# Performance work log

Measured on AMD Instinct MI355X. Metric: run time of the kernel, lower is better.

Reference implementation:

```python
import jax, jax.numpy as jnp
import numpy as np
import math

B, N, D = 2, 2048, 512   # batch, seq, input_dim
H = 8                     # num_head
DK, DV = 512, 512         # dim_k, dim_v (dim_v == input_dim for the final reshape)


def setup_inputs() -> dict:
    key = jax.random.key(0)
    ks = jax.random.split(key, 7)
    s = 1.0 / math.sqrt(D)
    return {
        "x":  jax.random.normal(ks[0], (B, N, D), jnp.float32),
        "Wq": jax.random.normal(ks[1], (H, DK, D), jnp.float32) * s,
        "bq": jax.random.normal(ks[2], (H, DK), jnp.float32) * s,
        "Wk": jax.random.normal(ks[3], (DK, D), jnp.float32) * s,
        "bk": jax.random.normal(ks[4], (DK,), jnp.float32) * s,
        "Wv": jax.random.normal(ks[5], (DV, D), jnp.float32) * s,
        "bv": jax.random.normal(ks[6], (DV,), jnp.float32) * s,
    }


def reference(x, Wq, bq, Wk, bk, Wv, bv):
    # Per-head Q projections (each head projects to full dim_k), batched as one einsum.
    Q = jnp.einsum("bnd,hkd->bhnk", x, Wq) + bq[None, :, None, :]   # [B,H,N,DK]
    K = x @ Wk.T + bk                                               # [B,N,DK] (shared)
    V = x @ Wv.T + bv                                               # [B,N,DV] (shared)
    scores = jnp.einsum("bhnk,bmk->bhnm", Q, K) / math.sqrt(DK)     # [B,H,N,N]
    A = jax.nn.softmax(scores, axis=-1)                             # softmax over keys
    At = jnp.swapaxes(A, -2, -1)                                    # quirk: transpose before V matmul
    out = jnp.einsum("bhnm,bnv->bhmv", A, V)                        # == At @ V (V broadcast over heads)
    out = out.reshape(-1, N, D)                                     # [B*H, N, D] since DV == D
    return (At, out)
```

## Files before the change

### kernel.cpp

```cpp
#include <hip/hip_runtime.h>
#include <stdint.h>

typedef __attribute__((ext_vector_type(8))) short short8;
typedef __attribute__((ext_vector_type(4))) float f4;
typedef unsigned short u16;

#define Nn 2048
#define Dd 512
#define Hh 8
#define BNrows 4096
#define SCALE 0.044194173824159216f

__device__ __forceinline__ u16 f2b(float f) {
  union { float f; uint32_t u; } c; c.f = f;
  uint32_t u = c.u;
  u += 0x7fffu + ((u >> 16) & 1u);
  return (u16)(u >> 16);
}

__device__ __forceinline__ void gload_lds16(const void* g, void* l) {
  __builtin_amdgcn_global_load_lds((const __attribute__((address_space(1))) void*)g,
                                   (__attribute__((address_space(3))) void*)l, 16, 0, 0);
}

__global__ void prep_kernel(const float* __restrict__ x,  u16* __restrict__ xb,
                            const float* __restrict__ Wq, u16* __restrict__ Wqb,
                            const float* __restrict__ Wk, u16* __restrict__ Wkb,
                            const float* __restrict__ Wv, u16* __restrict__ Wvb,
                            float* __restrict__ ssum) {
  const int g = blockIdx.x * 256 + threadIdx.x;
  if (g >= 589824) {
    ssum[g - 589824] = 0.0f;
    return;
  }
  const float* src; u16* dst; int i;
  if (g < 262144)      { src = x;  dst = xb;  i = g; }
  else if (g < 524288) { src = Wq; dst = Wqb; i = g - 262144; }
  else if (g < 557056) { src = Wk; dst = Wkb; i = g - 524288; }
  else                 { src = Wv; dst = Wvb; i = g - 557056; }
  const f4* s4 = (const f4*)src;
  f4 a = s4[2*i], b = s4[2*i+1];
  short8 o;
  o[0]=(short)f2b(a[0]); o[1]=(short)f2b(a[1]); o[2]=(short)f2b(a[2]); o[3]=(short)f2b(a[3]);
  o[4]=(short)f2b(b[0]); o[5]=(short)f2b(b[1]); o[6]=(short)f2b(b[2]); o[7]=(short)f2b(b[3]);
  ((short8*)dst)[i] = o;
}

__global__ void recip_kernel(const float* __restrict__ s, float* __restrict__ rs, int n) {
  int i = blockIdx.x * 256 + threadIdx.x;
  if (i < n) rs[i] = 1.0f / s[i];
}

__launch_bounds__(256)
__global__ void proj_all(const u16* __restrict__ xb, const u16* __restrict__ Wqb,
                         const u16* __restrict__ Wkb, const u16* __restrict__ Wvb,
                         const float* __restrict__ bq, const float* __restrict__ bk,
                         const float* __restrict__ bv,
                         u16* __restrict__ Qb, u16* __restrict__ Kb, u16* __restrict__ Vtb) {
  __shared__ __align__(16) u16 Al[128*64];
  __shared__ __align__(16) u16 Bl[128*64];
  const int bid = blockIdx.x;
  const u16 *A, *Bm; u16* C;
  const float* bias;
  int lda, ldb, ldc, bias_row, m0, n0;
  if (bid < 1024) {
    A = xb; lda = 512; Bm = Wqb; ldb = 512; bias = bq; bias_row = 0;
    C = Qb; ldc = 4096; n0 = (bid & 31) * 128; m0 = (bid >> 5) * 128;
  } else if (bid < 1152) {
    const int id = bid - 1024;
    A = xb; lda = 512; Bm = Wkb; ldb = 512; bias = bk; bias_row = 0;
    C = Kb; ldc = 512; n0 = (id & 3) * 128; m0 = (id >> 2) * 128;
  } else {
    const int id = bid - 1152;
    A = Wvb; lda = 512; Bm = xb; ldb = 512; bias = bv; bias_row = 1;
    C = Vtb; ldc = 4096; n0 = (id & 31) * 128; m0 = (id >> 5) * 128;
  }
  const int t = threadIdx.x, w = t >> 6, l = t & 63;
  const int wm = (w >> 1) * 64, wn = (w & 1) * 64;
  const int srow = l >> 3, scol = (l & 7) * 8;
  f4 acc[4][4] = {};
  for (int k0 = 0; k0 < 512; k0 += 64) {
    #pragma unroll
    for (int j = 0; j < 4; ++j) {
      const int chunk = (w << 2) + j;
      const int row = (chunk << 3) + srow;
      gload_lds16(A  + (size_t)(m0 + row) * lda + (k0 + scol), &Al[chunk << 9]);
      gload_lds16(Bm + (size_t)(n0 + row) * ldb + (k0 + scol), &Bl[chunk << 9]);
    }
    __syncthreads();
    #pragma unroll
    for (int ks = 0; ks < 64; ks += 32) {
      short8 af[4], bfr[4];
      #pragma unroll
      for (int i = 0; i < 4; ++i)
        af[i] = *(const short8*)&Al[(wm + i*16 + (l & 15)) * 64 + ks + ((l >> 4) << 3)];
      #pragma unroll
      for (int j = 0; j < 4; ++j)
        bfr[j] = *(const short8*)&Bl[(wn + j*16 + (l & 15)) * 64 + ks + ((l >> 4) << 3)];
      #pragma unroll
      for (int i = 0; i < 4; ++i)
        #pragma unroll
        for (int j = 0; j < 4; ++j)
          acc[i][j] = __builtin_amdgcn_mfma_f32_16x16x32_bf16(af[i], bfr[j], acc[i][j], 0, 0, 0);
    }
    __syncthreads();
  }
  const int cr = (l >> 4) << 2, cc = l & 15;
  #pragma unroll
  for (int i = 0; i < 4; ++i) {
    #pragma unroll
    for (int j = 0; j < 4; ++j) {
      const int col = n0 + wn + j*16 + cc;
      #pragma unroll
      for (int r = 0; r < 4; ++r) {
        const int row = m0 + wm + i*16 + cr + r;
        const float bb = bias_row ? bias[row] : bias[col];
        C[(size_t)row * ldc + col] = f2b(acc[i][j][r] + bb);
      }
    }
  }
}

__launch_bounds__(256)
__global__ void score_gemm(const u16* __restrict__ Kb, const u16* __restrict__ Qb,
                           float* __restrict__ E, float* __restrict__ ssum) {
  __shared__ __align__(16) u16 Al[128*64];
  __shared__ __align__(16) u16 Bl[128*64];
  const int t = threadIdx.x, w = t >> 6, l = t & 63;
  const int bh = blockIdx.z, b = bh >> 3, h = bh & 7;
  const u16* A  = Kb + (size_t)b * Nn * Dd;
  const u16* Bm = Qb + (size_t)b * Nn * BNrows + h * Dd;
  float* C = E + (size_t)bh * Nn * Nn;
  const int m0 = blockIdx.y * 128, n0 = blockIdx.x * 128;
  const int wm = (w >> 1) * 64, wn = (w & 1) * 64;
  const int srow = l >> 3, scol = (l & 7) * 8;
  f4 acc[4][4] = {};
  for (int k0 = 0; k0 < 512; k0 += 64) {
    #pragma unroll
    for (int j = 0; j < 4; ++j) {
      const int chunk = (w << 2) + j;
      const int row = (chunk << 3) + srow;
      gload_lds16(A  + (size_t)(m0 + row) * Dd      + (k0 + scol), &Al[chunk << 9]);
      gload_lds16(Bm + (size_t)(n0 + row) * BNrows  + (k0 + scol), &Bl[chunk << 9]);
    }
    __syncthreads();
    #pragma unroll
    for (int ks = 0; ks < 64; ks += 32) {
      short8 af[4], bfr[4];
      #pragma unroll
      for (int i = 0; i < 4; ++i)
        af[i] = *(const short8*)&Al[(wm + i*16 + (l & 15)) * 64 + ks + ((l >> 4) << 3)];
      #pragma unroll
      for (int j = 0; j < 4; ++j)
        bfr[j] = *(const short8*)&Bl[(wn + j*16 + (l & 15)) * 64 + ks + ((l >> 4) << 3)];
      #pragma unroll
      for (int i = 0; i < 4; ++i)
        #pragma unroll
        for (int j = 0; j < 4; ++j)
          acc[i][j] = __builtin_amdgcn_mfma_f32_16x16x32_bf16(af[i], bfr[j], acc[i][j], 0, 0, 0);
    }
    __syncthreads();
  }
  const int cr = (l >> 4) << 2, cc = l & 15;
  float psum[4] = {0.f, 0.f, 0.f, 0.f};
  #pragma unroll
  for (int i = 0; i < 4; ++i) {
    #pragma unroll
    for (int j = 0; j < 4; ++j) {
      const int col = n0 + wn + j*16 + cc;
      #pragma unroll
      for (int r = 0; r < 4; ++r) {
        const int row = m0 + wm + i*16 + cr + r;
        const float e = __expf(acc[i][j][r] * SCALE);
        C[(size_t)row * Nn + col] = e;
        psum[j] += e;
      }
    }
  }
  float* sp = ssum + bh * Nn + n0 + wn;
  #pragma unroll
  for (int j = 0; j < 4; ++j) {
    float p = psum[j];
    p += __shfl_xor(p, 16);
    p += __shfl_xor(p, 32);
    if (l < 16) atomicAdd(&sp[j*16 + l], p);
  }
}

__launch_bounds__(256)
__global__ void out_gemm(float* __restrict__ E, const u16* __restrict__ Vt,
                         const float* __restrict__ rs, float* __restrict__ O) {
  __shared__ __align__(16) u16 Al[64*32];
  __shared__ __align__(16) u16 Bl[512*32];
  const int t = threadIdx.x, w = t >> 6, l = t & 63;
  const int mb = blockIdx.x, bh = blockIdx.y, b = bh >> 3;
  float* Ep = E + (size_t)bh * Nn * Nn + (size_t)mb * 64 * Nn;
  const float* rsp = rs + bh * Nn;
  const u16* Vp = Vt + (size_t)b * Nn;
  const int wv = w << 7;
  const int am = t >> 2, an8 = (t & 3) << 3;
  const int bvr = l >> 2, bcol = (l & 3) << 3;
  f4 acc[4][8] = {};
  for (int k0 = 0; k0 < Nn; k0 += 32) {
    #pragma unroll
    for (int j = 0; j < 8; ++j) {
      const int chunk = (w << 3) + j;
      const int vrow = (chunk << 4) + bvr;
      gload_lds16(Vp + (size_t)vrow * BNrows + k0 + bcol, &Bl[chunk << 9]);
    }
    float* ap = Ep + (size_t)am * Nn + k0 + an8;
    f4 x0 = *(const f4*)ap;
    f4 x1 = *(const f4*)(ap + 4);
    const f4 r0 = *(const f4*)(rsp + k0 + an8);
    const f4 r1 = *(const f4*)(rsp + k0 + an8 + 4);
    x0 *= r0; x1 *= r1;
    *(f4*)ap = x0; *(f4*)(ap + 4) = x1;
    short8 ab;
    ab[0]=(short)f2b(x0[0]); ab[1]=(short)f2b(x0[1]); ab[2]=(short)f2b(x0[2]); ab[3]=(short)f2b(x0[3]);
    ab[4]=(short)f2b(x1[0]); ab[5]=(short)f2b(x1[1]); ab[6]=(short)f2b(x1[2]); ab[7]=(short)f2b(x1[3]);
    *(short8*)&Al[am * 32 + an8] = ab;
    __syncthreads();
    short8 af[4];
    #pragma unroll
    for (int i = 0; i < 4; ++i)
      af[i] = *(const short8*)&Al[(i*16 + (l & 15)) * 32 + ((l >> 4) << 3)];
    #pragma unroll
    for (int j = 0; j < 8; ++j) {
      const short8 bfj = *(const short8*)&Bl[(wv + j*16 + (l & 15)) * 32 + ((l >> 4) << 3)];
      #pragma unroll
      for (int i = 0; i < 4; ++i)
        acc[i][j] = __builtin_amdgcn_mfma_f32_16x16x32_bf16(af[i], bfj, acc[i][j], 0, 0, 0);
    }
    __syncthreads();
  }
  float* Op = O + (size_t)bh * Nn * Dd + (size_t)mb * 64 * Dd;
  #pragma unroll
  for (int i = 0; i < 4; ++i)
    #pragma unroll
    for (int j = 0; j < 8; ++j)
      #pragma unroll
      for (int r = 0; r < 4; ++r)
        Op[(size_t)(i*16 + ((l >> 4) << 2) + r) * Dd + (wv + j*16 + (l & 15))] = acc[i][j][r];
}

extern "C" void kernel_launch(void* const* d_in, const int* in_sizes, int n_in,
                              void* d_out, int out_size, void* d_ws, size_t ws_size,
                              hipStream_t stream) {
  const float* x  = (const float*)d_in[0];
  const float* Wq = (const float*)d_in[1];
  const float* bq = (const float*)d_in[2];
  const float* Wk = (const float*)d_in[3];
  const float* bk = (const float*)d_in[4];
  const float* Wv = (const float*)d_in[5];
  const float* bv = (const float*)d_in[6];

  u16* xb  = (u16*)d_ws;
  u16* Wqb = xb  + (size_t)4096 * 512;
  u16* Wkb = Wqb + (size_t)4096 * 512;
  u16* Wvb = Wkb + (size_t)512 * 512;
  u16* Qb  = Wvb + (size_t)512 * 512;
  u16* Kb  = Qb  + (size_t)4096 * 4096;
  u16* Vtb = Kb  + (size_t)4096 * 512;
  float* ssum = (float*)(Vtb + (size_t)4096 * 512);
  float* rs   = ssum + 16 * 2048;

  float* Eo = (float*)d_out;
  float* Oo = Eo + (size_t)16 * 2048 * 2048;

  prep_kernel<<<2432, 256, 0, stream>>>(x, xb, Wq, Wqb, Wk, Wkb, Wv, Wvb, ssum);
  proj_all<<<1280, 256, 0, stream>>>(xb, Wqb, Wkb, Wvb, bq, bk, bv, Qb, Kb, Vtb);
  score_gemm<<<dim3(16, 16, 16), 256, 0, stream>>>(Kb, Qb, Eo, ssum);
  recip_kernel<<<128, 256, 0, stream>>>(ssum, rs, 32768);
  out_gemm<<<dim3(32, 16), 256, 0, stream>>>(Eo, Vtb, rs, Oo);
}
```

Before: 687.2 us.

## Double-buffer out_gemm V tiles, prefetch E rows, and XOR-swizzle LDS layouts

Rewrites the out_gemm main loop as a software pipeline. The next V tile loads asynchronously into a second LDS buffer, and the next E/rowsum registers are fetched while the current tile is normalized and fed to MFMA. Both A and B LDS tiles use an XOR swizzle to cut bank conflicts, and the V-transpose producer writes in the matching swizzled order. Explicit waitcnt/barrier/setprio control replaces __syncthreads. Costs are a doubled B LDS footprint and a launch-bounds occupancy hint, plus correctness risk from the hand-tuned vmcnt count.

```diff
diff --git a/kernel.cpp b/kernel.cpp
--- a/kernel.cpp
+++ b/kernel.cpp
@@ -115,7 +115,11 @@
       for (int r = 0; r < 4; ++r) {
         const int row = m0 + wm + i*16 + cr + r;
         const float bb = bias_row ? bias[row] : bias[col];
-        C[(size_t)row * ldc + col] = f2b(acc[i][j][r] + bb);
+        int colw = col;
+        if (bias_row) {
+          colw = (col & ~31) | ((((col >> 3) & 3) ^ ((row >> 1) & 3)) << 3) | (col & 7);
+        }
+        C[(size_t)row * ldc + colw] = f2b(acc[i][j][r] + bb);
       }
     }
   }
@@ -187,11 +191,11 @@
   }
 }
 
-__launch_bounds__(256)
+__launch_bounds__(256, 2)
 __global__ void out_gemm(float* __restrict__ E, const u16* __restrict__ Vt,
                          const float* __restrict__ rs, float* __restrict__ O) {
+  __shared__ __align__(16) u16 Bl[2][512*32];
   __shared__ __align__(16) u16 Al[64*32];
-  __shared__ __align__(16) u16 Bl[512*32];
   const int t = threadIdx.x, w = t >> 6, l = t & 63;
   const int mb = blockIdx.x, bh = blockIdx.y, b = bh >> 3;
   float* Ep = E + (size_t)bh * Nn * Nn + (size_t)mb * 64 * Nn;
@@ -199,40 +203,76 @@
   const u16* Vp = Vt + (size_t)b * Nn;
   const int wv = w << 7;
   const int am = t >> 2, an8 = (t & 3) << 3;
-  const int bvr = l >> 2, bcol = (l & 3) << 3;
+  const int bvr = l >> 2, bg8 = (l & 3) << 3;
   f4 acc[4][8] = {};
-  for (int k0 = 0; k0 < Nn; k0 += 32) {
+
+  f4 e0, e1, r0, r1, e0n, e1n, r0n, r1n;
+  #pragma unroll
+  for (int j = 0; j < 8; ++j) {
+    const int chunk = (w << 3) + j;
+    const int vrow = (chunk << 4) + bvr;
+    gload_lds16(Vp + (size_t)vrow * BNrows + bg8, &Bl[0][chunk << 9]);
+  }
+  {
+    const float* ap = Ep + (size_t)am * Nn + an8;
+    e0 = *(const f4*)ap; e1 = *(const f4*)(ap + 4);
+    r0 = *(const f4*)(rsp + an8); r1 = *(const f4*)(rsp + an8 + 4);
+  }
+
+  for (int it = 0; it < 64; ++it) {
+    const int cur = it & 1;
+    const int kn = (it < 63) ? ((it + 1) << 5) : (63 << 5);
     #pragma unroll
     for (int j = 0; j < 8; ++j) {
       const int chunk = (w << 3) + j;
       const int vrow = (chunk << 4) + bvr;
-      gload_lds16(Vp + (size_t)vrow * BNrows + k0 + bcol, &Bl[chunk << 9]);
-    }
-    float* ap = Ep + (size_t)am * Nn + k0 + an8;
-    f4 x0 = *(const f4*)ap;
-    f4 x1 = *(const f4*)(ap + 4);
-    const f4 r0 = *(const f4*)(rsp + k0 + an8);
-    const f4 r1 = *(const f4*)(rsp + k0 + an8 + 4);
-    x0 *= r0; x1 *= r1;
-    *(f4*)ap = x0; *(f4*)(ap + 4) = x1;
-    short8 ab;
-    ab[0]=(short)f2b(x0[0]); ab[1]=(short)f2b(x0[1]); ab[2]=(short)f2b(x0[2]); ab[3]=(short)f2b(x0[3]);
-    ab[4]=(short)f2b(x1[0]); ab[5]=(short)f2b(x1[1]); ab[6]=(short)f2b(x1[2]); ab[7]=(short)f2b(x1[3]);
-    *(short8*)&Al[am * 32 + an8] = ab;
-    __syncthreads();
-    short8 af[4];
-    #pragma unroll
-    for (int i = 0; i < 4; ++i)
-      af[i] = *(const short8*)&Al[(i*16 + (l & 15)) * 32 + ((l >> 4) << 3)];
+      gload_lds16(Vp + (size_t)vrow * BNrows + kn + bg8, &Bl[cur ^ 1][chunk << 9]);
+    }
+    {
+      const float* apn = Ep + (size_t)am * Nn + kn + an8;
+      e0n = *(const f4*)apn; e1n = *(const f4*)(apn + 4);
+      r0n = *(const f4*)(rsp + kn + an8); r1n = *(const f4*)(rsp + kn + an8 + 4);
+    }
+    {
+      f4 x0 = e0 * r0, x1 = e1 * r1;
+      float* ap = Ep + (size_t)am * Nn + (it << 5) + an8;
+      *(f4*)ap = x0; *(f4*)(ap + 4) = x1;
+      short8 ab;
+      ab[0]=(short)f2b(x0[0]); ab[1]=(short)f2b(x0[1]); ab[2]=(short)f2b(x0[2]); ab[3]=(short)f2b(x0[3]);
+      ab[4]=(short)f2b(x1[0]); ab[5]=(short)f2b(x1[1]); ab[6]=(short)f2b(x1[2]); ab[7]=(short)f2b(x1[3]);
+      const int ag = (t & 3) ^ ((am >> 1) & 3);
+      *(short8*)&Al[am * 32 + (ag << 3)] = ab;
+    }
+    asm volatile("s_waitcnt lgkmcnt(0)" ::: "memory");
+    asm volatile("s_waitcnt vmcnt(12)" ::: "memory");
+    __builtin_amdgcn_s_barrier();
+    __builtin_amdgcn_sched_barrier(0);
+    short8 af[4], bf_[8];
+    #pragma unroll
+    for (int i = 0; i < 4; ++i) {
+      const int row = i*16 + (l & 15);
+      const int g = (l >> 4) ^ ((row >> 1) & 3);
+      af[i] = *(const short8*)&Al[row * 32 + (g << 3)];
+    }
     #pragma unroll
     for (int j = 0; j < 8; ++j) {
-      const short8 bfj = *(const short8*)&Bl[(wv + j*16 + (l & 15)) * 32 + ((l >> 4) << 3)];
-      #pragma unroll
-      for (int i = 0; i < 4; ++i)
-        acc[i][j] = __builtin_amdgcn_mfma_f32_16x16x32_bf16(af[i], bfj, acc[i][j], 0, 0, 0);
-    }
-    __syncthreads();
-  }
+      const int row = wv + j*16 + (l & 15);
+      const int g = (l >> 4) ^ ((row >> 1) & 3);
+      bf_[j] = *(const short8*)&Bl[cur][row * 32 + (g << 3)];
+    }
+    asm volatile("s_waitcnt lgkmcnt(0)" ::: "memory");
+    __builtin_amdgcn_s_barrier();
+    __builtin_amdgcn_sched_barrier(0);
+    __builtin_amdgcn_s_setprio(1);
+    #pragma unroll
+    for (int j = 0; j < 8; ++j)
+      #pragma unroll
+      for (int i = 0; i < 4; ++i)
+        acc[i][j] = __builtin_amdgcn_mfma_f32_16x16x32_bf16(af[i], bf_[j], acc[i][j], 0, 0, 0);
+    __builtin_amdgcn_s_setprio(0);
+    e0 = e0n; e1 = e1n; r0 = r0n; r1 = r1n;
+  }
+
   float* Op = O + (size_t)bh * Nn * Dd + (size_t)mb * 64 * Dd;
   #pragma unroll
   for (int i = 0; i < 4; ++i)
```

Result: no change. 698.1 us (+1.6%).
